# Kernel optimization log

Hardware: AMD Instinct MI355X
Metric: run time of the kernel (lower is better)

Reference implementation:

```python
import jax, jax.numpy as jnp
import numpy as np

MAX_TAG = 16          # tag ids live in [0, MAX_TAG]; 0 = background
NUM_SEG = MAX_TAG + 1
LGG_VALUE = 3.0


def setup_inputs() -> dict:
    key = jax.random.key(0)
    k1, k2, k3 = jax.random.split(key, 3)
    B, C, H, W = 16, 8, 512, 512
    gt_kernel_key = jax.random.randint(k1, (B, H, W), 0, MAX_TAG + 1, dtype=jnp.int32)
    training_mask = jax.random.randint(k2, (B, H, W), 0, 2, dtype=jnp.int32)
    similarity_vector = jax.random.normal(k3, (B, C, H, W), dtype=jnp.float32)
    return {
        "gt_kernel_key": gt_kernel_key,
        "training_mask": training_mask,
        "similarity_vector": similarity_vector,
    }


def _per_sample_loss(sim_hwc, gk, mask):
    # sim_hwc: [H, W, C]; gk, mask: [H, W]
    C = sim_hwc.shape[-1]
    flat_sim = sim_hwc.reshape(-1, C)            # [HW, C]
    flat_gk = gk.reshape(-1)                     # [HW]
    ones = jnp.ones_like(flat_gk, dtype=jnp.float32)

    # segment mean per tag over the UNMASKED kernel map (matches original:
    # tags are selected with the mask, but means use gt_kernel directly)
    sums = jax.ops.segment_sum(flat_sim, flat_gk, num_segments=NUM_SEG)      # [T, C]
    counts = jax.ops.segment_sum(ones, flat_gk, num_segments=NUM_SEG)       # [T]
    means = sums / jnp.maximum(counts, 1.0)[:, None]

    # a tag participates iff it appears in gt_kernel_key * training_mask and != 0
    masked_gk = flat_gk * mask.reshape(-1)
    masked_counts = jax.ops.segment_sum(ones, masked_gk, num_segments=NUM_SEG)
    present = (masked_counts > 0).at[0].set(False)                           # [T]

    # pairwise distances between tag means (tiny: NUM_SEG x NUM_SEG)
    diff = means[:, None, :] - means[None, :, :]                             # [T, T, C]
    dist = jnp.sqrt(jnp.sum(diff * diff, axis=-1) + 1e-12)                   # [T, T]
    pair_loss = jnp.log(jnp.maximum(LGG_VALUE - dist, 0.0) ** 2 + 1.0)

    valid = present[:, None] & present[None, :] & ~jnp.eye(NUM_SEG, dtype=bool)
    n_valid = jnp.sum(valid.astype(jnp.float32))
    loss = jnp.sum(jnp.where(valid, pair_loss, 0.0)) / jnp.maximum(n_valid, 1.0)
    sample_valid = (jnp.sum(present.astype(jnp.int32)) >= 2).astype(jnp.float32)
    return loss, sample_valid


def reference(gt_kernel_key, training_mask, similarity_vector):
    # [B, C, H, W] -> [B, H, W, C]
    sim = jnp.transpose(similarity_vector, (0, 2, 3, 1))
    losses, valids = jax.vmap(_per_sample_loss)(sim, gt_kernel_key, training_mask)
    n = jnp.sum(valids)
    return jnp.where(n > 0, jnp.sum(losses * valids) / jnp.maximum(n, 1.0), 0.0)
```

## Files before the change

kernel.cpp:

```cpp
#include <hip/hip_runtime.h>

#define NB 16
#define NC 8
#define HW (512*512)
#define NT 16
#define LGG 3.0f

#define BLOCKS 1024
#define THREADS 256
#define BPSAMP (BLOCKS/NB)
#define PXB (HW/BPSAMP)
#define TILE 512
#define NTILES (PXB/TILE)
#define JITERS 4
#define NCOL 10
#define ACCW (NT*NCOL)

#define GK_OFF  0
#define MK_OFF  2048
#define SIM_OFF 4096
#define BUF_BYTES 20480
#define LDS_BYTES (2*BUF_BYTES)

typedef __attribute__((ext_vector_type(8))) short bf16x8;
typedef __attribute__((ext_vector_type(4))) float f32x4;

__device__ __forceinline__ unsigned pk_bf16(float x, float y) {
    unsigned r;
    asm("v_cvt_pk_bf16_f32 %0, %1, %2" : "=v"(r) : "v"(x), "v"(y));
    return r;
}
__device__ __forceinline__ unsigned onehot2(int a, int b, int r1) {
    return (a == r1 ? 0x3F80u : 0u) | (b == r1 ? 0x3F800000u : 0u);
}
__device__ __forceinline__ unsigned mask2(int a, int b) {
    return (a ? 0x3F80u : 0u) | (b ? 0x3F800000u : 0u);
}
__device__ __forceinline__ void gload_lds16(const void* g, void* lds) {
    __builtin_amdgcn_global_load_lds(
        (const __attribute__((address_space(1))) void*)g,
        (__attribute__((address_space(3))) void*)lds, 16, 0, 0);
}

__device__ __forceinline__ void stage(const char* gkB, const char* mkB,
                                      const char* smB, char* buf,
                                      int t0b, int wid, int lane) {
    #pragma unroll
    for (int k = 0; k < 5; ++k) {
        const int idx = wid + 4 * k;
        const char* src; int dst;
        if (idx < 2) {
            src = gkB + t0b + idx * 1024 + lane * 16;
            dst = GK_OFF + idx * 1024 + lane * 16;
        } else if (idx < 4) {
            src = mkB + t0b + (idx - 2) * 1024 + lane * 16;
            dst = MK_OFF + (idx - 2) * 1024 + lane * 16;
        } else {
            const int s = idx - 4, p = s >> 1, h = s & 1;
            const int local = h * 1024 + lane * 16;
            const int goff = (local - 16 * p) & 2047;
            src = smB + (size_t)p * (HW * 4) + t0b + goff;
            dst = SIM_OFF + p * 2048 + local;
        }
        gload_lds16(src, buf + dst);
    }
}

__global__ __launch_bounds__(256) void init_ws(float* g_acc) {
    const int i = threadIdx.x;
    #pragma unroll
    for (int k = 0; k < NB*ACCW; k += 256)
        if (k + i < NB*ACCW) g_acc[k + i] = 0.f;
}

__global__ __launch_bounds__(THREADS) void accum(
    const int* __restrict__ gk, const int* __restrict__ mask,
    const float* __restrict__ sim, float* __restrict__ g_acc)
{
    const int tid  = threadIdx.x;
    const int lane = tid & 63, wid = tid >> 6;
    const int bid  = blockIdx.x;
    const int b    = bid / BPSAMP;
    const int sb   = bid % BPSAMP;
    const int c    = lane & 15;
    const int l4   = lane >> 4;
    const int base = sb * PXB;

    __shared__ __align__(16) char lds[LDS_BYTES];

    const char* gkB = (const char*)(gk   + (size_t)b * HW + base);
    const char* mkB = (const char*)(mask + (size_t)b * HW + base);
    const char* smB = (const char*)(sim  + (size_t)b * NC * HW + base);

    f32x4 acc = {0.f, 0.f, 0.f, 0.f};
    const int r1 = c + 1;
    const int pl = c & 7;
    const int rot = 16 * pl;

    stage(gkB, mkB, smB, lds, 0, wid, lane);

    #pragma unroll 1
    for (int t = 0; t < NTILES; ++t) {
        char* cur = lds + (t & 1) * BUF_BYTES;
        if (t + 1 < NTILES) {
            stage(gkB, mkB, smB, lds + ((t + 1) & 1) * BUF_BYTES,
                  (t + 1) * (TILE * 4), wid, lane);
            asm volatile("s_waitcnt vmcnt(5)" ::: "memory");
        } else {
            asm volatile("s_waitcnt vmcnt(0)" ::: "memory");
        }
        __builtin_amdgcn_sched_barrier(0);
        __builtin_amdgcn_s_barrier();

        #pragma unroll
        for (int j = 0; j < JITERS; ++j) {
            const int o = (wid * 128 + j * 32 + l4 * 8) * 4;
            const int4 g0 = *(const int4*)(cur + GK_OFF + o);
            const int4 g1 = *(const int4*)(cur + GK_OFF + o + 16);
            float4 v0 = {0,0,0,0}, v1 = {0,0,0,0};
            if (c < 8) {
                const char* sp = cur + SIM_OFF + pl * 2048;
                v0 = *(const float4*)(sp + ((o + rot) & 2047));
                v1 = *(const float4*)(sp + ((o + 16 + rot) & 2047));
            }
            int4 m0 = {0,0,0,0}, m1 = {0,0,0,0};
            if (c == 9) {
                m0 = *(const int4*)(cur + MK_OFF + o);
                m1 = *(const int4*)(cur + MK_OFF + o + 16);
            }

            union { bf16x8 v; unsigned u[4]; } A, B;
            A.u[0] = onehot2(g0.x, g0.y, r1);
            A.u[1] = onehot2(g0.z, g0.w, r1);
            A.u[2] = onehot2(g1.x, g1.y, r1);
            A.u[3] = onehot2(g1.z, g1.w, r1);
            const unsigned bs0 = pk_bf16(v0.x, v0.y), bs1 = pk_bf16(v0.z, v0.w);
            const unsigned bs2 = pk_bf16(v1.x, v1.y), bs3 = pk_bf16(v1.z, v1.w);
            const unsigned bm0 = mask2(m0.x, m0.y), bm1 = mask2(m0.z, m0.w);
            const unsigned bm2 = mask2(m1.x, m1.y), bm3 = mask2(m1.z, m1.w);
            B.u[0] = c < 8 ? bs0 : (c == 8 ? 0x3F803F80u : (c == 9 ? bm0 : 0u));
            B.u[1] = c < 8 ? bs1 : (c == 8 ? 0x3F803F80u : (c == 9 ? bm1 : 0u));
            B.u[2] = c < 8 ? bs2 : (c == 8 ? 0x3F803F80u : (c == 9 ? bm2 : 0u));
            B.u[3] = c < 8 ? bs3 : (c == 8 ? 0x3F803F80u : (c == 9 ? bm3 : 0u));

            acc = __builtin_amdgcn_mfma_f32_16x16x32_bf16(A.v, B.v, acc, 0, 0, 0);
        }
        __builtin_amdgcn_s_barrier();
    }

    float* lred = (float*)lds;
    const int row0 = l4 * 4;
    #pragma unroll
    for (int i = 0; i < 4; ++i) lred[wid * 256 + (row0 + i) * 16 + c] = acc[i];
    __syncthreads();

    if (tid < NT * NCOL) {
        const int r = tid / NCOL, cc = tid % NCOL;
        const float s = lred[0*256 + r*16 + cc] + lred[1*256 + r*16 + cc]
                      + lred[2*256 + r*16 + cc] + lred[3*256 + r*16 + cc];
        atomicAdd(&g_acc[b * ACCW + tid], s);
    }
}

__global__ __launch_bounds__(256) void finalize(
    const float* __restrict__ g_acc, float* __restrict__ out)
{
    __shared__ float    means[NB][NT][NC];
    __shared__ unsigned pres[NB];
    __shared__ float    sl[NB], sn[NB];
    const int tid = threadIdx.x;

    if (tid < NB) pres[tid] = 0u;
    __syncthreads();

    {
        const int b = tid >> 4, t = tid & 15;
        const float* row = g_acc + b * ACCW + t * NCOL;
        const float cnt = row[8];
        const float mc  = row[9];
        const float inv = 1.f / fmaxf(cnt, 1.f);
        #pragma unroll
        for (int cc = 0; cc < NC; ++cc) means[b][t][cc] = row[cc] * inv;
        if (mc > 0.5f) atomicOr(&pres[b], 1u << (t + 1));
    }
    __syncthreads();

    const int b = tid >> 4, i = tid & 15;
    const unsigned pr = pres[b];
    float loss = 0.f, nv = 0.f;
    if ((pr >> (i + 1)) & 1u) {
        #pragma unroll
        for (int j = 0; j < NT; ++j) {
            if (j != i && ((pr >> (j + 1)) & 1u)) {
                float d2 = 0.f;
                #pragma unroll
                for (int cc = 0; cc < NC; ++cc) {
                    const float d = means[b][i][cc] - means[b][j][cc];
                    d2 += d * d;
                }
                const float dist = sqrtf(d2 + 1e-12f);
                const float r = fmaxf(LGG - dist, 0.f);
                loss += logf(r * r + 1.f);
                nv += 1.f;
            }
        }
    }
    #pragma unroll
    for (int o = 8; o; o >>= 1) { loss += __shfl_xor(loss, o); nv += __shfl_xor(nv, o); }
    if (i == 0) {
        const float v = (__popc(pr) >= 2) ? 1.f : 0.f;
        sl[b] = v * (loss / fmaxf(nv, 1.f));
        sn[b] = v;
    }
    __syncthreads();
    if (tid == 0) {
        float tl = 0.f, tv = 0.f;
        for (int bb = 0; bb < NB; ++bb) { tl += sl[bb]; tv += sn[bb]; }
        out[0] = (tv > 0.f) ? tl / tv : 0.f;
    }
}

extern "C" void kernel_launch(void* const* d_in, const int* in_sizes, int n_in,
                              void* d_out, int out_size, void* d_ws, size_t ws_size,
                              hipStream_t stream) {
    const int*   gk   = (const int*)d_in[0];
    const int*   mask = (const int*)d_in[1];
    const float* sim  = (const float*)d_in[2];
    float* out   = (float*)d_out;
    float* g_acc = (float*)d_ws;

    init_ws<<<1, 256, 0, stream>>>(g_acc);
    accum<<<BLOCKS, THREADS, 0, stream>>>(gk, mask, sim, g_acc);
    finalize<<<1, 256, 0, stream>>>(g_acc, out);
}
```

Before: 44.70 us.

## Replace atomic accumulation with per-block partial sums and drop init kernel

The accumulation kernel now uses 512-thread blocks with eight waves and 1024-pixel tiles, halving the block count. Each block writes its own partial sums to workspace instead of issuing atomicAdds, which removes the zero-init kernel launch. A 1024-thread finalize kernel, one wave per sample, reduces the per-block partials and computes the pairwise loss. This removes one launch and atomic contention, at the cost of a serial partial-sum reduction in finalize and larger LDS use per block.

```diff
diff --git a/kernel.cpp b/kernel.cpp
--- a/kernel.cpp
+++ b/kernel.cpp
@@ -6,20 +6,21 @@
 #define NT 16
 #define LGG 3.0f
 
-#define BLOCKS 1024
-#define THREADS 256
+#define BLOCKS 512
+#define THREADS 512
+#define WPB 8
 #define BPSAMP (BLOCKS/NB)
 #define PXB (HW/BPSAMP)
-#define TILE 512
+#define TILE 1024
 #define NTILES (PXB/TILE)
 #define JITERS 4
 #define NCOL 10
 #define ACCW (NT*NCOL)
 
 #define GK_OFF  0
-#define MK_OFF  2048
-#define SIM_OFF 4096
-#define BUF_BYTES 20480
+#define MK_OFF  4096
+#define SIM_OFF 8192
+#define BUF_BYTES 40960
 #define LDS_BYTES (2*BUF_BYTES)
 
 typedef __attribute__((ext_vector_type(8))) short bf16x8;
@@ -47,35 +48,28 @@
                                       int t0b, int wid, int lane) {
     #pragma unroll
     for (int k = 0; k < 5; ++k) {
-        const int idx = wid + 4 * k;
+        const int idx = wid + 8 * k;
         const char* src; int dst;
-        if (idx < 2) {
+        if (idx < 4) {
             src = gkB + t0b + idx * 1024 + lane * 16;
             dst = GK_OFF + idx * 1024 + lane * 16;
-        } else if (idx < 4) {
-            src = mkB + t0b + (idx - 2) * 1024 + lane * 16;
-            dst = MK_OFF + (idx - 2) * 1024 + lane * 16;
+        } else if (idx < 8) {
+            src = mkB + t0b + (idx - 4) * 1024 + lane * 16;
+            dst = MK_OFF + (idx - 4) * 1024 + lane * 16;
         } else {
-            const int s = idx - 4, p = s >> 1, h = s & 1;
+            const int s = idx - 8, p = s >> 2, h = s & 3;
             const int local = h * 1024 + lane * 16;
-            const int goff = (local - 16 * p) & 2047;
+            const int goff = (local - 16 * p) & 4095;
             src = smB + (size_t)p * (HW * 4) + t0b + goff;
-            dst = SIM_OFF + p * 2048 + local;
+            dst = SIM_OFF + p * 4096 + local;
         }
         gload_lds16(src, buf + dst);
     }
-}
-
-__global__ __launch_bounds__(256) void init_ws(float* g_acc) {
-    const int i = threadIdx.x;
-    #pragma unroll
-    for (int k = 0; k < NB*ACCW; k += 256)
-        if (k + i < NB*ACCW) g_acc[k + i] = 0.f;
 }
 
 __global__ __launch_bounds__(THREADS) void accum(
     const int* __restrict__ gk, const int* __restrict__ mask,
-    const float* __restrict__ sim, float* __restrict__ g_acc)
+    const float* __restrict__ sim, float* __restrict__ psum)
 {
     const int tid  = threadIdx.x;
     const int lane = tid & 63, wid = tid >> 6;
@@ -119,9 +113,9 @@
             const int4 g1 = *(const int4*)(cur + GK_OFF + o + 16);
             float4 v0 = {0,0,0,0}, v1 = {0,0,0,0};
             if (c < 8) {
-                const char* sp = cur + SIM_OFF + pl * 2048;
-                v0 = *(const float4*)(sp + ((o + rot) & 2047));
-                v1 = *(const float4*)(sp + ((o + 16 + rot) & 2047));
+                const char* sp = cur + SIM_OFF + pl * 4096;
+                v0 = *(const float4*)(sp + ((o + rot) & 4095));
+                v1 = *(const float4*)(sp + ((o + 16 + rot) & 4095));
             }
             int4 m0 = {0,0,0,0}, m1 = {0,0,0,0};
             if (c == 9) {
@@ -154,69 +148,80 @@
     for (int i = 0; i < 4; ++i) lred[wid * 256 + (row0 + i) * 16 + c] = acc[i];
     __syncthreads();
 
-    if (tid < NT * NCOL) {
+    if (tid < ACCW) {
         const int r = tid / NCOL, cc = tid % NCOL;
-        const float s = lred[0*256 + r*16 + cc] + lred[1*256 + r*16 + cc]
-                      + lred[2*256 + r*16 + cc] + lred[3*256 + r*16 + cc];
-        atomicAdd(&g_acc[b * ACCW + tid], s);
-    }
-}
-
-__global__ __launch_bounds__(256) void finalize(
-    const float* __restrict__ g_acc, float* __restrict__ out)
+        float s = 0.f;
+        #pragma unroll
+        for (int w = 0; w < WPB; ++w) s += lred[w * 256 + r * 16 + cc];
+        psum[(size_t)bid * ACCW + tid] = s;
+    }
+}
+
+__global__ __launch_bounds__(1024) void finalize(
+    const float* __restrict__ psum, float* __restrict__ out)
 {
-    __shared__ float    means[NB][NT][NC];
-    __shared__ unsigned pres[NB];
-    __shared__ float    sl[NB], sn[NB];
+    __shared__ float Sw[NB][ACCW];
+    __shared__ float means_s[NB][NT][NC];
+    __shared__ float sl[NB], sn[NB];
     const int tid = threadIdx.x;
-
-    if (tid < NB) pres[tid] = 0u;
+    const int w = tid >> 6, lane = tid & 63;
+
+    {
+        const float* base = psum + (size_t)w * BPSAMP * ACCW;
+        float a0 = 0.f, a1 = 0.f, a2 = 0.f;
+        #pragma unroll 4
+        for (int s = 0; s < BPSAMP; ++s) {
+            a0 += base[s * ACCW + lane];
+            a1 += base[s * ACCW + lane + 64];
+            if (lane < 32) a2 += base[s * ACCW + lane + 128];
+        }
+        Sw[w][lane] = a0; Sw[w][lane + 64] = a1;
+        if (lane < 32) Sw[w][lane + 128] = a2;
+    }
+
+    #pragma unroll
+    for (int k = 0; k < 2; ++k) {
+        const int idx = lane + 64 * k;
+        const int t = idx >> 3, cc = idx & 7;
+        means_s[w][t][cc] = Sw[w][t * NCOL + cc]
+                            / fmaxf(Sw[w][t * NCOL + 8], 1.f);
+    }
+    const unsigned long long bal =
+        __ballot(lane < NT && (Sw[w][lane * NCOL + 9] > 0.5f));
+    const unsigned pres = (unsigned)(bal & 0xFFFFull);
+
+    float loss = 0.f, nv = 0.f;
+    #pragma unroll
+    for (int k = 0; k < 4; ++k) {
+        const int pid = lane + 64 * k;
+        const int i = pid >> 4, j = pid & 15;
+        if (i != j && ((pres >> i) & 1u) && ((pres >> j) & 1u)) {
+            float d2 = 0.f;
+            #pragma unroll
+            for (int cc = 0; cc < NC; ++cc) {
+                const float d = means_s[w][i][cc] - means_s[w][j][cc];
+                d2 += d * d;
+            }
+            const float dist = sqrtf(d2 + 1e-12f);
+            const float r = fmaxf(LGG - dist, 0.f);
+            loss += logf(r * r + 1.f);
+            nv += 1.f;
+        }
+    }
+    #pragma unroll
+    for (int o = 32; o; o >>= 1) { loss += __shfl_xor(loss, o); nv += __shfl_xor(nv, o); }
+    if (lane == 0) {
+        const float v = (__popc(pres) >= 2) ? 1.f : 0.f;
+        sl[w] = v * (loss / fmaxf(nv, 1.f));
+        sn[w] = v;
+    }
     __syncthreads();
-
-    {
-        const int b = tid >> 4, t = tid & 15;
-        const float* row = g_acc + b * ACCW + t * NCOL;
-        const float cnt = row[8];
-        const float mc  = row[9];
-        const float inv = 1.f / fmaxf(cnt, 1.f);
+    if (tid < 64) {
+        float l = (tid < NB) ? sl[tid] : 0.f;
+        float v = (tid < NB) ? sn[tid] : 0.f;
         #pragma unroll
-        for (int cc = 0; cc < NC; ++cc) means[b][t][cc] = row[cc] * inv;
-        if (mc > 0.5f) atomicOr(&pres[b], 1u << (t + 1));
-    }
-    __syncthreads();
-
-    const int b = tid >> 4, i = tid & 15;
-    const unsigned pr = pres[b];
-    float loss = 0.f, nv = 0.f;
-    if ((pr >> (i + 1)) & 1u) {
-        #pragma unroll
-        for (int j = 0; j < NT; ++j) {
-            if (j != i && ((pr >> (j + 1)) & 1u)) {
-                float d2 = 0.f;
-                #pragma unroll
-                for (int cc = 0; cc < NC; ++cc) {
-                    const float d = means[b][i][cc] - means[b][j][cc];
-                    d2 += d * d;
-                }
-                const float dist = sqrtf(d2 + 1e-12f);
-                const float r = fmaxf(LGG - dist, 0.f);
-                loss += logf(r * r + 1.f);
-                nv += 1.f;
-            }
-        }
-    }
-    #pragma unroll
-    for (int o = 8; o; o >>= 1) { loss += __shfl_xor(loss, o); nv += __shfl_xor(nv, o); }
-    if (i == 0) {
-        const float v = (__popc(pr) >= 2) ? 1.f : 0.f;
-        sl[b] = v * (loss / fmaxf(nv, 1.f));
-        sn[b] = v;
-    }
-    __syncthreads();
-    if (tid == 0) {
-        float tl = 0.f, tv = 0.f;
-        for (int bb = 0; bb < NB; ++bb) { tl += sl[bb]; tv += sn[bb]; }
-        out[0] = (tv > 0.f) ? tl / tv : 0.f;
+        for (int o = 8; o; o >>= 1) { l += __shfl_xor(l, o); v += __shfl_xor(v, o); }
+        if (tid == 0) out[0] = (v > 0.f) ? l / v : 0.f;
     }
 }
 
@@ -226,10 +231,9 @@
     const int*   gk   = (const int*)d_in[0];
     const int*   mask = (const int*)d_in[1];
     const float* sim  = (const float*)d_in[2];
-    float* out   = (float*)d_out;
-    float* g_acc = (float*)d_ws;
-
-    init_ws<<<1, 256, 0, stream>>>(g_acc);
-    accum<<<BLOCKS, THREADS, 0, stream>>>(gk, mask, sim, g_acc);
-    finalize<<<1, 256, 0, stream>>>(g_acc, out);
-}
+    float* out  = (float*)d_out;
+    float* psum = (float*)d_ws;
+
+    accum<<<BLOCKS, THREADS, 0, stream>>>(gk, mask, sim, psum);
+    finalize<<<1, 1024, 0, stream>>>(psum, out);
+}
```

Result: slower. 47.85 us (+7.0%).
